# Kernel tuning notes

Hardware: AMD Instinct MI355X
Metric: run time of the kernel (lower is better)

Reference implementation:

```python
import jax, jax.numpy as jnp
import numpy as np

EPS = 1e-5

def conv3x3(x, w, b, stride=1):
    y = jax.lax.conv_general_dilated(x, w, (stride, stride), 'SAME',
                                     dimension_numbers=('NCHW', 'OIHW', 'NCHW'))
    return y + b[None, :, None, None]

def batchnorm_train(x, gamma, beta):
    # training-mode BN: batch statistics over (N, H, W)
    mean = x.mean(axis=(0, 2, 3), keepdims=True)
    var = x.var(axis=(0, 2, 3), keepdims=True)
    xh = (x - mean) * jax.lax.rsqrt(var + EPS)
    return xh * gamma[None, :, None, None] + beta[None, :, None, None]

def haar_dwt2(x):
    # pywt.dwt2(x, 'db1') on last two axes; even H,W so 'symmetric' padding is a no-op.
    # a = (x0 + x1)/sqrt2, d = (x0 - x1)/sqrt2 per axis -> 2x2 block combinations / 2.
    x00 = x[:, :, 0::2, 0::2]
    x01 = x[:, :, 0::2, 1::2]
    x10 = x[:, :, 1::2, 0::2]
    x11 = x[:, :, 1::2, 1::2]
    cA = (x00 + x01 + x10 + x11) * 0.5
    cH = (x00 + x01 - x10 - x11) * 0.5  # pywt 'da': detail along rows
    cV = (x00 - x01 + x10 - x11) * 0.5  # pywt 'ad': detail along cols
    cD = (x00 - x01 - x10 + x11) * 0.5
    return cA, cH, cV, cD


def setup_inputs() -> dict:
    key = jax.random.key(0)
    ks = jax.random.split(key, 8)
    N, in_c, out_c, H, W = 4, 3, 64, 512, 512

    def kaiming(k, shape):
        fan_in = shape[1] * shape[2] * shape[3]
        return jax.random.normal(k, shape, jnp.float32) * np.sqrt(2.0 / fan_in)

    inputs = jax.random.normal(ks[0], (N, in_c, H, W), jnp.float32)
    return {
        'inputs': inputs,
        # conv_block: conv1 -> bn1 -> conv2 -> bn2 -> relu
        'w1': kaiming(ks[1], (out_c, in_c, 3, 3)),
        'b1': jnp.zeros((out_c,), jnp.float32),
        'g1': jnp.ones((out_c,), jnp.float32),
        'be1': jnp.zeros((out_c,), jnp.float32),
        'w2': kaiming(ks[2], (out_c, out_c, 3, 3)),
        'b2': jnp.zeros((out_c,), jnp.float32),
        'g2': jnp.ones((out_c,), jnp.float32),
        'be2': jnp.zeros((out_c,), jnp.float32),
        # conv_dwt_block: conv(out_c*4 -> out_c) -> bn -> relu
        'w3': kaiming(ks[3], (out_c, out_c * 4, 3, 3)),
        'b3': jnp.zeros((out_c,), jnp.float32),
        'g3': jnp.ones((out_c,), jnp.float32),
        'be3': jnp.zeros((out_c,), jnp.float32),
    }


def reference(inputs, w1, b1, g1, be1, w2, b2, g2, be2, w3, b3, g3, be3):
    # conv_block
    x = conv3x3(inputs, w1, b1)
    x = batchnorm_train(x, g1, be1)
    x = conv3x3(x, w2, b2)
    x = batchnorm_train(x, g2, be2)
    skip_con = jax.nn.relu(x)

    # original detaches skip_con before the (CPU pywt) DWT -> no grad through this branch
    dwt_in = jax.lax.stop_gradient(skip_con)
    cA, cH, cV, cD = haar_dwt2(dwt_in)
    dwt = jnp.concatenate((cA, cH, cV, cD), axis=1)  # [N, 4*out_c, H/2, W/2]

    y = conv3x3(dwt, w3, b3)
    y = batchnorm_train(y, g3, be3)
    dwt_out = jax.nn.relu(y)
    return dwt_out, skip_con
```

## Files before the change

### kernel.cpp

```cpp
#include <hip/hip_runtime.h>
#include <cstdint>

typedef float f32x4 __attribute__((ext_vector_type(4)));
typedef __bf16 bf16x8 __attribute__((ext_vector_type(8)));
typedef unsigned int uint32;
typedef unsigned short ushort_t;

__device__ __forceinline__ ushort_t f2bf(float f) {
    uint32 u = __builtin_bit_cast(uint32, f);
    u = (u + 0x7fffu + ((u >> 16) & 1u)) >> 16;
    return (ushort_t)u;
}
__device__ __forceinline__ float bf2f(ushort_t h) {
    return __builtin_bit_cast(float, (uint32)h << 16);
}

__device__ __forceinline__ void gload_lds16(const void* g, void* l) {
    __builtin_amdgcn_global_load_lds(
        (const __attribute__((address_space(1))) uint32*)g,
        (__attribute__((address_space(3))) uint32*)l, 16, 0, 0);
}

__global__ __launch_bounds__(256) void im2col1_kernel(
    const float* __restrict__ in,
    ushort_t* __restrict__ P)
{
    int px = blockIdx.x * 256 + threadIdx.x;
    int n = px >> 18, rem = px & 262143;
    int y = rem >> 9, x = rem & 511;
    ushort_t pv[32];
#pragma unroll
    for (int ci = 0; ci < 3; ++ci)
#pragma unroll
        for (int t = 0; t < 9; ++t) {
            int dy = t / 3 - 1, dx = t % 3 - 1;
            int yy = y + dy, xx = x + dx;
            bool v = ((unsigned)yy < 512u) && ((unsigned)xx < 512u);
            pv[ci * 9 + t] = v ? f2bf(in[((n * 3 + ci) * 512 + yy) * 512 + xx])
                               : (ushort_t)0;
        }
#pragma unroll
    for (int k = 27; k < 32; ++k) pv[k] = 0;
    uint4* dst = (uint4*)(P + (size_t)px * 32);
    dst[0] = *(uint4*)(pv);
    dst[1] = *(uint4*)(pv + 8);
    dst[2] = *(uint4*)(pv + 16);
    dst[3] = *(uint4*)(pv + 24);
}

__global__ void prepw1_kernel(const float* __restrict__ w1,
                              ushort_t* __restrict__ Wsw1)
{
    int i = blockIdx.x * 256 + threadIdx.x;
    int ii = i & 7, lane = (i >> 3) & 63, nt = i >> 9;
    int cout = nt * 16 + (lane & 15);
    int k = (lane >> 4) * 8 + ii;
    Wsw1[i] = (k < 27) ? f2bf(w1[cout * 27 + k]) : (ushort_t)0;
}

__global__ __launch_bounds__(256) void gemm1_kernel(
    const ushort_t* __restrict__ P,
    const ushort_t* __restrict__ Wsw1,
    const float* __restrict__ b1,
    ushort_t* __restrict__ X1,
    float* __restrict__ stats)
{
    __shared__ float sred[4][128];
    int tid = threadIdx.x;
    int wave = tid >> 6, lane = tid & 63;
    int lp = lane & 15, lg = lane >> 4;
    int pxb = blockIdx.x * 256 + wave * 64;

    bf16x8 wf[4];
#pragma unroll
    for (int nt = 0; nt < 4; ++nt)
        wf[nt] = *(const bf16x8*)(Wsw1 + (nt * 64 + lane) * 8);

    f32x4 acc[4][4];
#pragma unroll
    for (int a = 0; a < 4; ++a)
#pragma unroll
        for (int b = 0; b < 4; ++b) acc[a][b] = (f32x4){0.f, 0.f, 0.f, 0.f};

#pragma unroll
    for (int nf = 0; nf < 4; ++nf) {
        bf16x8 bfrag = *(const bf16x8*)(P + (size_t)(pxb + nf * 16 + lp) * 32 + lg * 8);
#pragma unroll
        for (int nt = 0; nt < 4; ++nt)
            acc[nt][nf] = __builtin_amdgcn_mfma_f32_16x16x32_bf16(
                wf[nt], bfrag, acc[nt][nf], 0, 0, 0);
    }

    float s16[16], q16[16];
#pragma unroll
    for (int j = 0; j < 16; ++j) { s16[j] = 0.f; q16[j] = 0.f; }

#pragma unroll
    for (int nf = 0; nf < 4; ++nf) {
        size_t px = (size_t)pxb + nf * 16 + lp;
#pragma unroll
        for (int nt = 0; nt < 4; ++nt) {
            ushort_t ov[4];
#pragma unroll
            for (int r = 0; r < 4; ++r) {
                float o = acc[nt][nf][r] + b1[nt * 16 + lg * 4 + r];
                s16[nt * 4 + r] += o;
                q16[nt * 4 + r] += o * o;
                ov[r] = f2bf(o);
            }
            *(ushort4*)(X1 + px * 64 + nt * 16 + lg * 4) = *(ushort4*)ov;
        }
    }

#pragma unroll
    for (int off = 1; off < 16; off <<= 1)
#pragma unroll
        for (int j = 0; j < 16; ++j) {
            s16[j] += __shfl_xor(s16[j], off);
            q16[j] += __shfl_xor(q16[j], off);
        }
    if (lp == 0) {
#pragma unroll
        for (int nt = 0; nt < 4; ++nt)
#pragma unroll
            for (int r = 0; r < 4; ++r) {
                int ch = nt * 16 + lg * 4 + r;
                sred[wave][ch]      = s16[nt * 4 + r];
                sred[wave][64 + ch] = q16[nt * 4 + r];
            }
    }
    __syncthreads();
    if (tid < 128) {
        float tot = sred[0][tid] + sred[1][tid] + sred[2][tid] + sred[3][tid];
        atomicAdd(&stats[(blockIdx.x & 31) * 128 + tid], tot);
    }
}

__global__ void finalize_kernel(const float* __restrict__ stats,
                                const float* __restrict__ gamma,
                                const float* __restrict__ beta,
                                float inv_cnt, float* __restrict__ scsh)
{
    int c = threadIdx.x;
    float S = 0.f, Q = 0.f;
    for (int b = 0; b < 32; ++b) {
        S += stats[b * 128 + c];
        Q += stats[b * 128 + 64 + c];
    }
    float mean = S * inv_cnt;
    float var  = Q * inv_cnt - mean * mean;
    float rs   = rsqrtf(var + 1e-5f);
    float sc   = gamma[c] * rs;
    scsh[c]      = sc;
    scsh[64 + c] = beta[c] - mean * sc;
}

__global__ __launch_bounds__(256) void prepw_kernel(
    const float* __restrict__ w, const float* __restrict__ scale,
    ushort_t* __restrict__ Wsw, int CIN)
{
    int i = blockIdx.x * 256 + threadIdx.x;
    int KC = CIN >> 5;
    int ii = i & 7, lane = (i >> 3) & 63, nt = (i >> 9) & 3;
    int rest = i >> 11;
    int kc = rest % KC, t = rest / KC;
    if (t >= 9) return;
    int cout = nt * 16 + (lane & 15);
    int cin  = kc * 32 + (lane >> 4) * 8 + ii;
    float v = w[(cout * CIN + cin) * 9 + t];
    if (scale) v *= scale[cin];
    Wsw[i] = f2bf(v);
}

__global__ void prepT_kernel(const float* __restrict__ w2,
                             const float* __restrict__ shift,
                             float* __restrict__ T)
{
    int idx = threadIdx.x;
    if (idx < 576) {
        int t = idx / 64, cout = idx % 64;
        float s = 0.f;
        for (int cin = 0; cin < 64; ++cin)
            s += w2[(cout * 64 + cin) * 9 + t] * shift[cin];
        T[idx] = s;
    }
    __syncthreads();
    if (idx < 64) {
        float s = 0.f;
        for (int t = 0; t < 9; ++t) s += T[t * 64 + idx];
        T[576 + idx] = s;
    }
}

template <int CIN, bool HAS_T, int HH, int WW>
__global__ __launch_bounds__(256, 3) void conv_mfma5_kernel(
    const ushort_t* __restrict__ X,
    const ushort_t* __restrict__ Wsw,
    const float* __restrict__ T,
    const float* __restrict__ bias,
    ushort_t* __restrict__ Y,
    float* __restrict__ stats)
{
    constexpr int KC     = CIN >> 5;
    constexpr int COLS_B = WW >> 6;
    constexpr int ROWS_B = HH >> 2;

    __shared__ ushort_t tiles[2][12672];

    int nwg = gridDim.x;
    int bid = blockIdx.x;
    int cpx = nwg >> 3;
    int bs  = (bid & 7) * cpx + (bid >> 3);

    int tid  = threadIdx.x;
    int wave = tid >> 6, lane = tid & 63;
    int lp = lane & 15, lg = lane >> 4;

    int tmp = bs;
    int ctile = tmp % COLS_B;  tmp /= COLS_B;
    int rtile = tmp % ROWS_B;
    int n     = tmp / ROWS_B;
    int y0 = rtile << 2, x0 = ctile << 6;
    int y  = y0 + wave;

    uint32 goff[7];
    uint32 vmask = 0;
#pragma unroll
    for (int j = 0; j < 7; ++j) {
        int s = tid + j * 256;
        goff[j] = 0;
        if (s < 1584) {
            int plane = s / 396;
            int px    = s - plane * 396;
            int ry    = px / 66;
            int cx    = px - ry * 66;
            int gy = y0 - 1 + ry, gx = x0 - 1 + cx;
            if (((unsigned)gy < (unsigned)HH) && ((unsigned)gx < (unsigned)WW)) {
                vmask |= (1u << j);
                goff[j] = (uint32)((((uint32)(n * HH + gy) * WW + gx) * CIN
                                    + plane * 8) * 2);
            } else {
                uint4 zz; zz.x = zz.y = zz.z = zz.w = 0u;
                *(uint4*)((char*)tiles[0] + s * 16) = zz;
                *(uint4*)((char*)tiles[1] + s * 16) = zz;
            }
        }
    }

    const char* Xb = (const char*)X;
    auto stage = [&](int c, int b) {
        uint32 cofs = (uint32)c * 64u;
#pragma unroll
        for (int j = 0; j < 7; ++j) {
            if (vmask & (1u << j))
                gload_lds16(Xb + goff[j] + cofs,
                            (char*)tiles[b] + j * 4096 + wave * 1024);
        }
    };

    f32x4 acc[4][4];
#pragma unroll
    for (int a = 0; a < 4; ++a)
#pragma unroll
        for (int b = 0; b < 4; ++b) acc[a][b] = (f32x4){0.f, 0.f, 0.f, 0.f};

    stage(0, 0);
    __syncthreads();

#pragma unroll 1
    for (int c = 0; c < KC; ++c) {
        if (c + 1 < KC) stage(c + 1, (c + 1) & 1);
        const ushort_t* tile = tiles[c & 1];

#pragma unroll
        for (int t = 0; t < 9; ++t) {
            const int dy = t / 3 - 1, dx = t % 3 - 1;
            bf16x8 wf[4];
#pragma unroll
            for (int nt = 0; nt < 4; ++nt)
                wf[nt] = *(const bf16x8*)(Wsw + (size_t)(((t * KC + c) << 2) + nt) * 512 + lane * 8);
            int prow = (wave + 1 + dy) * 66 + (1 + dx) + lp;
#pragma unroll
            for (int nf = 0; nf < 4; ++nf) {
                int px = prow + nf * 16;
                bf16x8 bfrag = *(const bf16x8*)(tile + lg * 3168 + px * 8);
#pragma unroll
                for (int nt = 0; nt < 4; ++nt)
                    acc[nt][nf] = __builtin_amdgcn_mfma_f32_16x16x32_bf16(
                        wf[nt], bfrag, acc[nt][nf], 0, 0, 0);
            }
        }
        __syncthreads();
    }

    float (*sred)[128] = (float(*)[128])tiles[0];

    bool top = (y == 0), bot = (y == HH - 1);
    float s16[16], q16[16];
#pragma unroll
    for (int j = 0; j < 16; ++j) { s16[j] = 0.f; q16[j] = 0.f; }

    size_t rowbase = ((size_t)(n * HH + y) * WW) * 64;
#pragma unroll
    for (int nf = 0; nf < 4; ++nf) {
        int x = x0 + nf * 16 + lp;
        bool lft = (x == 0), rgt = (x == WW - 1);
        bool edge = top | bot | lft | rgt;
#pragma unroll
        for (int nt = 0; nt < 4; ++nt) {
            ushort_t ov[4];
#pragma unroll
            for (int r = 0; r < 4; ++r) {
                int ch = nt * 16 + lg * 4 + r;
                float o = acc[nt][nf][r] + bias[ch];
                if (HAS_T) {
                    o += T[576 + ch];
                    if (edge) {
#pragma unroll
                        for (int t = 0; t < 9; ++t) {
                            int dy = t / 3 - 1, dx = t % 3 - 1;
                            bool miss = (top && dy < 0) || (bot && dy > 0) ||
                                        (lft && dx < 0) || (rgt && dx > 0);
                            if (miss) o -= T[t * 64 + ch];
                        }
                    }
                }
                s16[nt * 4 + r] += o;
                q16[nt * 4 + r] += o * o;
                ov[r] = f2bf(o);
            }
            *(ushort4*)(Y + rowbase + (size_t)x * 64 + nt * 16 + lg * 4) = *(ushort4*)ov;
        }
    }

#pragma unroll
    for (int off = 1; off < 16; off <<= 1)
#pragma unroll
        for (int j = 0; j < 16; ++j) {
            s16[j] += __shfl_xor(s16[j], off);
            q16[j] += __shfl_xor(q16[j], off);
        }
    if (lp == 0) {
#pragma unroll
        for (int nt = 0; nt < 4; ++nt)
#pragma unroll
            for (int r = 0; r < 4; ++r) {
                int ch = nt * 16 + lg * 4 + r;
                sred[wave][ch]      = s16[nt * 4 + r];
                sred[wave][64 + ch] = q16[nt * 4 + r];
            }
    }
    __syncthreads();
    if (tid < 128) {
        float tot = sred[0][tid] + sred[1][tid] + sred[2][tid] + sred[3][tid];
        atomicAdd(&stats[(bs & 31) * 128 + tid], tot);
    }
}

__global__ __launch_bounds__(256) void bn2_dwt_skip_kernel(
    const ushort_t* __restrict__ X2, const float* __restrict__ scsh,
    float* __restrict__ skip,
    ushort_t* __restrict__ X3)
{
    __shared__ float v[128][65];
    int tid = threadIdx.x;
    int b = blockIdx.x;
    int n  = b >> 11;
    int r2 = b & 2047;
    int y0 = (r2 >> 3) << 1;
    int x0 = (r2 & 7) << 6;

#pragma unroll
    for (int k = 0; k < 4; ++k) {
        int q  = tid + k * 256;
        int px = q >> 3;
        int cb = (q & 7) * 8;
        int gy = y0 + (px >> 6);
        int gx = x0 + (px & 63);
        uint4 raw = *(const uint4*)(X2 + ((size_t)(n * 512 + gy) * 512 + gx) * 64 + cb);
        const ushort_t* up = (const ushort_t*)&raw;
#pragma unroll
        for (int j = 0; j < 8; ++j) {
            float f = bf2f(up[j]);
            float o = f * scsh[cb + j] + scsh[64 + cb + j];
            v[px][cb + j] = fmaxf(o, 0.f);
        }
    }
    __syncthreads();

    {
        int c = tid >> 2, sub = tid & 3;
#pragma unroll
        for (int rr = 0; rr < 2; ++rr) {
            float* orow = skip + ((size_t)(n * 64 + c) * 512 + (y0 + rr)) * 512 + x0;
#pragma unroll
            for (int qq = 0; qq < 4; ++qq) {
                int xb = qq * 16 + sub * 4;
                float4 w4;
                w4.x = v[rr * 64 + xb + 0][c];
                w4.y = v[rr * 64 + xb + 1][c];
                w4.z = v[rr * 64 + xb + 2][c];
                w4.w = v[rr * 64 + xb + 3][c];
                *(float4*)(orow + xb) = w4;
            }
        }
    }
    {
        int c = tid & 63, jj = tid >> 6;
        int yq = y0 >> 1, xq = x0 >> 1;
#pragma unroll
        for (int it = 0; it < 8; ++it) {
            int xl = jj * 8 + it;
            float x00 = v[2 * xl][c],      x01 = v[2 * xl + 1][c];
            float x10 = v[64 + 2 * xl][c], x11 = v[64 + 2 * xl + 1][c];
            float cA = (x00 + x01 + x10 + x11) * 0.5f;
            float cH = (x00 + x01 - x10 - x11) * 0.5f;
            float cV = (x00 - x01 + x10 - x11) * 0.5f;
            float cD = (x00 - x01 - x10 + x11) * 0.5f;
            ushort_t* dst = X3 + ((size_t)(n * 256 + yq) * 256 + xq + xl) * 256 + c;
            dst[0]   = f2bf(cA);
            dst[64]  = f2bf(cH);
            dst[128] = f2bf(cV);
            dst[192] = f2bf(cD);
        }
    }
}

__global__ __launch_bounds__(256) void bn3_kernel(
    const ushort_t* __restrict__ X4, const float* __restrict__ scsh,
    float* __restrict__ out)
{
    __shared__ float v[64][65];
    int tid = threadIdx.x;
    int b = blockIdx.x;
    int n  = b >> 10;
    int r2 = b & 1023;
    int y  = r2 >> 2;
    int x0 = (r2 & 3) << 6;

#pragma unroll
    for (int k = 0; k < 2; ++k) {
        int q  = tid + k * 256;
        int px = q >> 3;
        int cb = (q & 7) * 8;
        uint4 raw = *(const uint4*)(X4 + ((size_t)(n * 256 + y) * 256 + x0 + px) * 64 + cb);
        const ushort_t* up = (const ushort_t*)&raw;
#pragma unroll
        for (int j = 0; j < 8; ++j) {
            float f = bf2f(up[j]);
            float o = f * scsh[cb + j] + scsh[64 + cb + j];
            v[px][cb + j] = fmaxf(o, 0.f);
        }
    }
    __syncthreads();
    int c = tid >> 2, sub = tid & 3;
    float* orow = out + ((size_t)(n * 64 + c) * 256 + y) * 256 + x0;
#pragma unroll
    for (int qq = 0; qq < 4; ++qq) {
        int xb = qq * 16 + sub * 4;
        float4 w4;
        w4.x = v[xb + 0][c];
        w4.y = v[xb + 1][c];
        w4.z = v[xb + 2][c];
        w4.w = v[xb + 3][c];
        *(float4*)(orow + xb) = w4;
    }
}

extern "C" void kernel_launch(void* const* d_in, const int* in_sizes, int n_in,
                              void* d_out, int out_size, void* d_ws, size_t ws_size,
                              hipStream_t stream)
{
    const float* in  = (const float*)d_in[0];
    const float* w1  = (const float*)d_in[1];
    const float* b1  = (const float*)d_in[2];
    const float* g1  = (const float*)d_in[3];
    const float* be1 = (const float*)d_in[4];
    const float* w2  = (const float*)d_in[5];
    const float* b2  = (const float*)d_in[6];
    const float* g2  = (const float*)d_in[7];
    const float* be2 = (const float*)d_in[8];
    const float* w3  = (const float*)d_in[9];
    const float* b3  = (const float*)d_in[10];
    const float* g3  = (const float*)d_in[11];
    const float* be3 = (const float*)d_in[12];

    float* out     = (float*)d_out;
    float* dwt_out = out;
    float* skip    = out + 16777216;

    char* ws = (char*)d_ws;
    ushort_t* X1 = (ushort_t*)ws;
    ushort_t* X2 = (ushort_t*)(ws + 134217728);
    ushort_t* P  = X2;
    ushort_t* X3 = X1;
    ushort_t* X4 = X2;
    char* aux = ws + 268435456;
    float* stats1 = (float*)(aux);
    float* stats2 = (float*)(aux + 16384);
    float* stats3 = (float*)(aux + 32768);
    float* scsh1  = (float*)(aux + 49152);
    float* scsh2  = (float*)(aux + 49664);
    float* scsh3  = (float*)(aux + 50176);
    float* T2     = (float*)(aux + 50688);
    ushort_t* Wsw2 = (ushort_t*)(aux + 57344);
    ushort_t* Wsw3 = (ushort_t*)(aux + 131072);
    ushort_t* Wsw1 = (ushort_t*)(aux + 425984);

    hipMemsetAsync(aux, 0, 49152, stream);

    im2col1_kernel<<<4096, 256, 0, stream>>>(in, P);
    prepw1_kernel<<<8, 256, 0, stream>>>(w1, Wsw1);
    gemm1_kernel<<<4096, 256, 0, stream>>>(P, Wsw1, b1, X1, stats1);
    finalize_kernel<<<1, 64, 0, stream>>>(stats1, g1, be1, 1.f / 1048576.f, scsh1);
    prepw_kernel<<<144, 256, 0, stream>>>(w2, scsh1, Wsw2, 64);
    prepT_kernel<<<1, 576, 0, stream>>>(w2, scsh1 + 64, T2);

    conv_mfma5_kernel<64, true, 512, 512><<<4096, 256, 0, stream>>>(
        X1, Wsw2, T2, b2, X2, stats2);
    finalize_kernel<<<1, 64, 0, stream>>>(stats2, g2, be2, 1.f / 1048576.f, scsh2);

    bn2_dwt_skip_kernel<<<8192, 256, 0, stream>>>(X2, scsh2, skip, X3);

    prepw_kernel<<<576, 256, 0, stream>>>(w3, nullptr, Wsw3, 256);
    conv_mfma5_kernel<256, false, 256, 256><<<1024, 256, 0, stream>>>(
        X3, Wsw3, nullptr, b3, X4, stats3);
    finalize_kernel<<<1, 64, 0, stream>>>(stats3, g3, be3, 1.f / 262144.f, scsh3);

    bn3_kernel<<<4096, 256, 0, stream>>>(X4, scsh3, dwt_out);
}
```

Measured before the change: 594.1 us.

## Split conv tile into 2 rows by 2 channel halves, preload weights per chunk

The conv kernel now covers 2 output rows per block instead of 4. Each row is split between two waves, and each wave handles half of the 64 output channels. This shrinks the LDS tile and the accumulators, which should help occupancy, and doubles the grid. All nine taps' weight fragments are now loaded into registers before the stage of the next chunk is issued, instead of reloading weights per tap. The cost is more halo reloads per output row and duplicated B-fragment LDS reads across the channel halves.

Result: no change. 586.0 us (-1.4%).

```diff
diff --git a/kernel.cpp b/kernel.cpp
--- a/kernel.cpp
+++ b/kernel.cpp
@@ -193,7 +193,7 @@
 }
 
 template <int CIN, bool HAS_T, int HH, int WW>
-__global__ __launch_bounds__(256, 3) void conv_mfma5_kernel(
+__global__ __launch_bounds__(256, 3) void conv_mfma6_kernel(
     const ushort_t* __restrict__ X,
     const ushort_t* __restrict__ Wsw,
     const float* __restrict__ T,
@@ -203,9 +203,9 @@
 {
     constexpr int KC     = CIN >> 5;
     constexpr int COLS_B = WW >> 6;
-    constexpr int ROWS_B = HH >> 2;
-
-    __shared__ ushort_t tiles[2][12672];
+    constexpr int ROWS_B = HH >> 1;
+
+    __shared__ ushort_t tiles[2][8448];
 
     int nwg = gridDim.x;
     int bid = blockIdx.x;
@@ -215,23 +215,24 @@
     int tid  = threadIdx.x;
     int wave = tid >> 6, lane = tid & 63;
     int lp = lane & 15, lg = lane >> 4;
+    int row = wave >> 1, h = wave & 1;
 
     int tmp = bs;
     int ctile = tmp % COLS_B;  tmp /= COLS_B;
     int rtile = tmp % ROWS_B;
     int n     = tmp / ROWS_B;
-    int y0 = rtile << 2, x0 = ctile << 6;
-    int y  = y0 + wave;
-
-    uint32 goff[7];
+    int y0 = rtile << 1, x0 = ctile << 6;
+    int y  = y0 + row;
+
+    uint32 goff[5];
     uint32 vmask = 0;
 #pragma unroll
-    for (int j = 0; j < 7; ++j) {
+    for (int j = 0; j < 5; ++j) {
         int s = tid + j * 256;
         goff[j] = 0;
-        if (s < 1584) {
-            int plane = s / 396;
-            int px    = s - plane * 396;
+        if (s < 1056) {
+            int plane = s / 264;
+            int px    = s - plane * 264;
             int ry    = px / 66;
             int cx    = px - ry * 66;
             int gy = y0 - 1 + ry, gx = x0 - 1 + cx;
@@ -251,16 +252,16 @@
     auto stage = [&](int c, int b) {
         uint32 cofs = (uint32)c * 64u;
 #pragma unroll
-        for (int j = 0; j < 7; ++j) {
+        for (int j = 0; j < 5; ++j) {
             if (vmask & (1u << j))
                 gload_lds16(Xb + goff[j] + cofs,
                             (char*)tiles[b] + j * 4096 + wave * 1024);
         }
     };
 
-    f32x4 acc[4][4];
-#pragma unroll
-    for (int a = 0; a < 4; ++a)
+    f32x4 acc[2][4];
+#pragma unroll
+    for (int a = 0; a < 2; ++a)
 #pragma unroll
         for (int b = 0; b < 4; ++b) acc[a][b] = (f32x4){0.f, 0.f, 0.f, 0.f};
 
@@ -269,25 +270,29 @@
 
 #pragma unroll 1
     for (int c = 0; c < KC; ++c) {
+        bf16x8 wreg[9][2];
+#pragma unroll
+        for (int t = 0; t < 9; ++t)
+#pragma unroll
+            for (int ntl = 0; ntl < 2; ++ntl)
+                wreg[t][ntl] = *(const bf16x8*)(
+                    Wsw + (size_t)(((t * KC + c) << 2) + (h * 2 + ntl)) * 512 + lane * 8);
+        __builtin_amdgcn_sched_barrier(0);
         if (c + 1 < KC) stage(c + 1, (c + 1) & 1);
+
         const ushort_t* tile = tiles[c & 1];
-
 #pragma unroll
         for (int t = 0; t < 9; ++t) {
             const int dy = t / 3 - 1, dx = t % 3 - 1;
-            bf16x8 wf[4];
-#pragma unroll
-            for (int nt = 0; nt < 4; ++nt)
-                wf[nt] = *(const bf16x8*)(Wsw + (size_t)(((t * KC + c) << 2) + nt) * 512 + lane * 8);
-            int prow = (wave + 1 + dy) * 66 + (1 + dx) + lp;
+            int prow = (row + 1 + dy) * 66 + (1 + dx) + lp;
 #pragma unroll
             for (int nf = 0; nf < 4; ++nf) {
                 int px = prow + nf * 16;
-                bf16x8 bfrag = *(const bf16x8*)(tile + lg * 3168 + px * 8);
-#pragma unroll
-                for (int nt = 0; nt < 4; ++nt)
-                    acc[nt][nf] = __builtin_amdgcn_mfma_f32_16x16x32_bf16(
-                        wf[nt], bfrag, acc[nt][nf], 0, 0, 0);
+                bf16x8 bfrag = *(const bf16x8*)(tile + lg * 2112 + px * 8);
+                acc[0][nf] = __builtin_amdgcn_mfma_f32_16x16x32_bf16(
+                    wreg[t][0], bfrag, acc[0][nf], 0, 0, 0);
+                acc[1][nf] = __builtin_amdgcn_mfma_f32_16x16x32_bf16(
+                    wreg[t][1], bfrag, acc[1][nf], 0, 0, 0);
             }
         }
         __syncthreads();
@@ -296,9 +301,9 @@
     float (*sred)[128] = (float(*)[128])tiles[0];
 
     bool top = (y == 0), bot = (y == HH - 1);
-    float s16[16], q16[16];
-#pragma unroll
-    for (int j = 0; j < 16; ++j) { s16[j] = 0.f; q16[j] = 0.f; }
+    float s8[8], q8[8];
+#pragma unroll
+    for (int j = 0; j < 8; ++j) { s8[j] = 0.f; q8[j] = 0.f; }
 
     size_t rowbase = ((size_t)(n * HH + y) * WW) * 64;
 #pragma unroll
@@ -307,12 +312,12 @@
         bool lft = (x == 0), rgt = (x == WW - 1);
         bool edge = top | bot | lft | rgt;
 #pragma unroll
-        for (int nt = 0; nt < 4; ++nt) {
+        for (int ntl = 0; ntl < 2; ++ntl) {
             ushort_t ov[4];
 #pragma unroll
             for (int r = 0; r < 4; ++r) {
-                int ch = nt * 16 + lg * 4 + r;
-                float o = acc[nt][nf][r] + bias[ch];
+                int ch = (h * 2 + ntl) * 16 + lg * 4 + r;
+                float o = acc[ntl][nf][r] + bias[ch];
                 if (HAS_T) {
                     o += T[576 + ch];
                     if (edge) {
@@ -325,34 +330,37 @@
                         }
                     }
                 }
-                s16[nt * 4 + r] += o;
-                q16[nt * 4 + r] += o * o;
+                s8[ntl * 4 + r] += o;
+                q8[ntl * 4 + r] += o * o;
                 ov[r] = f2bf(o);
             }
-            *(ushort4*)(Y + rowbase + (size_t)x * 64 + nt * 16 + lg * 4) = *(ushort4*)ov;
+            *(ushort4*)(Y + rowbase + (size_t)x * 64 + (h * 2 + ntl) * 16 + lg * 4)
+                = *(ushort4*)ov;
         }
     }
 
 #pragma unroll
     for (int off = 1; off < 16; off <<= 1)
 #pragma unroll
-        for (int j = 0; j < 16; ++j) {
-            s16[j] += __shfl_xor(s16[j], off);
-            q16[j] += __shfl_xor(q16[j], off);
+        for (int j = 0; j < 8; ++j) {
+            s8[j] += __shfl_xor(s8[j], off);
+            q8[j] += __shfl_xor(q8[j], off);
         }
     if (lp == 0) {
 #pragma unroll
-        for (int nt = 0; nt < 4; ++nt)
+        for (int ntl = 0; ntl < 2; ++ntl)
 #pragma unroll
             for (int r = 0; r < 4; ++r) {
-                int ch = nt * 16 + lg * 4 + r;
-                sred[wave][ch]      = s16[nt * 4 + r];
-                sred[wave][64 + ch] = q16[nt * 4 + r];
+                int ch = (h * 2 + ntl) * 16 + lg * 4 + r;
+                sred[wave][ch]      = s8[ntl * 4 + r];
+                sred[wave][64 + ch] = q8[ntl * 4 + r];
             }
     }
     __syncthreads();
     if (tid < 128) {
-        float tot = sred[0][tid] + sred[1][tid] + sred[2][tid] + sred[3][tid];
+        int ch = tid & 63;
+        int h2 = ch >> 5;
+        float tot = sred[h2][tid] + sred[2 + h2][tid];
         atomicAdd(&stats[(bs & 31) * 128 + tid], tot);
     }
 }
@@ -516,14 +524,14 @@
     prepw_kernel<<<144, 256, 0, stream>>>(w2, scsh1, Wsw2, 64);
     prepT_kernel<<<1, 576, 0, stream>>>(w2, scsh1 + 64, T2);
 
-    conv_mfma5_kernel<64, true, 512, 512><<<4096, 256, 0, stream>>>(
+    conv_mfma6_kernel<64, true, 512, 512><<<8192, 256, 0, stream>>>(
         X1, Wsw2, T2, b2, X2, stats2);
     finalize_kernel<<<1, 64, 0, stream>>>(stats2, g2, be2, 1.f / 1048576.f, scsh2);
 
     bn2_dwt_skip_kernel<<<8192, 256, 0, stream>>>(X2, scsh2, skip, X3);
 
     prepw_kernel<<<576, 256, 0, stream>>>(w3, nullptr, Wsw3, 256);
-    conv_mfma5_kernel<256, false, 256, 256><<<1024, 256, 0, stream>>>(
+    conv_mfma6_kernel<256, false, 256, 256><<<2048, 256, 0, stream>>>(
         X3, Wsw3, nullptr, b3, X4, stats3);
     finalize_kernel<<<1, 64, 0, stream>>>(stats3, g3, be3, 1.f / 262144.f, scsh3);
 
```

## Stage conv weights into LDS alongside activation tiles with dynamic shared memory

Applied to the files above, without the earlier changes.

The conv kernel now loads weight fragments for each input-channel chunk into double-buffered LDS using global_load_lds, instead of reading them per wave from global memory. Shared memory becomes dynamic (about 124 KB) and launch bounds drop to one block per CU. The aim is to cut repeated global/L2 weight traffic and its latency inside the MFMA loop. The cost is much lower occupancy, which leaves less latency hiding for the activation loads.

Result: slower. 750.6 us (+26.3%).

```diff
diff --git a/kernel.cpp b/kernel.cpp
--- a/kernel.cpp
+++ b/kernel.cpp
@@ -193,7 +193,7 @@
 }
 
 template <int CIN, bool HAS_T, int HH, int WW>
-__global__ __launch_bounds__(256, 3) void conv_mfma5_kernel(
+__global__ __launch_bounds__(256, 1) void conv_mfma7_kernel(
     const ushort_t* __restrict__ X,
     const ushort_t* __restrict__ Wsw,
     const float* __restrict__ T,
@@ -205,7 +205,7 @@
     constexpr int COLS_B = WW >> 6;
     constexpr int ROWS_B = HH >> 2;
 
-    __shared__ ushort_t tiles[2][12672];
+    extern __shared__ char smem[];
 
     int nwg = gridDim.x;
     int bid = blockIdx.x;
@@ -215,6 +215,7 @@
     int tid  = threadIdx.x;
     int wave = tid >> 6, lane = tid & 63;
     int lp = lane & 15, lg = lane >> 4;
+    int wbase16 = (tid & 192) * 16;
 
     int tmp = bs;
     int ctile = tmp % COLS_B;  tmp /= COLS_B;
@@ -223,12 +224,12 @@
     int y0 = rtile << 2, x0 = ctile << 6;
     int y  = y0 + wave;
 
-    uint32 goff[7];
-    uint32 vmask = 0;
+    uint32 agoff[7];
+    uint32 amask = 0;
 #pragma unroll
     for (int j = 0; j < 7; ++j) {
         int s = tid + j * 256;
-        goff[j] = 0;
+        agoff[j] = 0;
         if (s < 1584) {
             int plane = s / 396;
             int px    = s - plane * 396;
@@ -236,25 +237,33 @@
             int cx    = px - ry * 66;
             int gy = y0 - 1 + ry, gx = x0 - 1 + cx;
             if (((unsigned)gy < (unsigned)HH) && ((unsigned)gx < (unsigned)WW)) {
-                vmask |= (1u << j);
-                goff[j] = (uint32)((((uint32)(n * HH + gy) * WW + gx) * CIN
-                                    + plane * 8) * 2);
+                amask |= (1u << j);
+                agoff[j] = (uint32)((((uint32)(n * HH + gy) * WW + gx) * CIN
+                                     + plane * 8) * 2);
             } else {
                 uint4 zz; zz.x = zz.y = zz.z = zz.w = 0u;
-                *(uint4*)((char*)tiles[0] + s * 16) = zz;
-                *(uint4*)((char*)tiles[1] + s * 16) = zz;
-            }
-        }
-    }
-
+                *(uint4*)(smem + s * 16)         = zz;
+                *(uint4*)(smem + 25344 + s * 16) = zz;
+            }
+        }
+    }
     const char* Xb = (const char*)X;
-    auto stage = [&](int c, int b) {
-        uint32 cofs = (uint32)c * 64u;
+    const char* Wb = (const char*)Wsw;
+
+    auto stage = [&](int c) {
+        char* ab = smem + (c & 1) * 25344;
+        char* wb = smem + 50688 + (c & 1) * 36864;
+        uint32 ca = (uint32)c * 64u;
+        uint32 cw = (uint32)c * 4096u;
 #pragma unroll
         for (int j = 0; j < 7; ++j) {
-            if (vmask & (1u << j))
-                gload_lds16(Xb + goff[j] + cofs,
-                            (char*)tiles[b] + j * 4096 + wave * 1024);
+            if (amask & (1u << j))
+                gload_lds16(Xb + agoff[j] + ca, ab + j * 4096 + wbase16);
+        }
+#pragma unroll
+        for (int j = 0; j < 9; ++j) {
+            gload_lds16(Wb + (uint32)(j * KC) * 4096u + cw + (uint32)tid * 16u,
+                        wb + j * 4096 + wbase16);
         }
     };
 
@@ -264,13 +273,14 @@
 #pragma unroll
         for (int b = 0; b < 4; ++b) acc[a][b] = (f32x4){0.f, 0.f, 0.f, 0.f};
 
-    stage(0, 0);
+    stage(0);
     __syncthreads();
 
 #pragma unroll 1
     for (int c = 0; c < KC; ++c) {
-        if (c + 1 < KC) stage(c + 1, (c + 1) & 1);
-        const ushort_t* tile = tiles[c & 1];
+        if (c + 1 < KC) stage(c + 1);
+        const char* ab = smem + (c & 1) * 25344;
+        const char* wb = smem + 50688 + (c & 1) * 36864;
 
 #pragma unroll
         for (int t = 0; t < 9; ++t) {
@@ -278,12 +288,12 @@
             bf16x8 wf[4];
 #pragma unroll
             for (int nt = 0; nt < 4; ++nt)
-                wf[nt] = *(const bf16x8*)(Wsw + (size_t)(((t * KC + c) << 2) + nt) * 512 + lane * 8);
+                wf[nt] = *(const bf16x8*)(wb + ((t * 4 + nt) * 64 + lane) * 16);
             int prow = (wave + 1 + dy) * 66 + (1 + dx) + lp;
 #pragma unroll
             for (int nf = 0; nf < 4; ++nf) {
                 int px = prow + nf * 16;
-                bf16x8 bfrag = *(const bf16x8*)(tile + lg * 3168 + px * 8);
+                bf16x8 bfrag = *(const bf16x8*)(ab + lg * 6336 + px * 16);
 #pragma unroll
                 for (int nt = 0; nt < 4; ++nt)
                     acc[nt][nf] = __builtin_amdgcn_mfma_f32_16x16x32_bf16(
@@ -293,7 +303,7 @@
         __syncthreads();
     }
 
-    float (*sred)[128] = (float(*)[128])tiles[0];
+    float (*sred)[128] = (float(*)[128])(smem + 50688);
 
     bool top = (y == 0), bot = (y == HH - 1);
     float s16[16], q16[16];
@@ -507,6 +517,14 @@
     ushort_t* Wsw3 = (ushort_t*)(aux + 131072);
     ushort_t* Wsw1 = (ushort_t*)(aux + 425984);
 
+    constexpr int kSmem = 124416;
+    hipFuncSetAttribute(
+        reinterpret_cast<const void*>(&conv_mfma7_kernel<64, true, 512, 512>),
+        hipFuncAttributeMaxDynamicSharedMemorySize, kSmem);
+    hipFuncSetAttribute(
+        reinterpret_cast<const void*>(&conv_mfma7_kernel<256, false, 256, 256>),
+        hipFuncAttributeMaxDynamicSharedMemorySize, kSmem);
+
     hipMemsetAsync(aux, 0, 49152, stream);
 
     im2col1_kernel<<<4096, 256, 0, stream>>>(in, P);
@@ -516,14 +534,14 @@
     prepw_kernel<<<144, 256, 0, stream>>>(w2, scsh1, Wsw2, 64);
     prepT_kernel<<<1, 576, 0, stream>>>(w2, scsh1 + 64, T2);
 
-    conv_mfma5_kernel<64, true, 512, 512><<<4096, 256, 0, stream>>>(
+    conv_mfma7_kernel<64, true, 512, 512><<<4096, 256, kSmem, stream>>>(
         X1, Wsw2, T2, b2, X2, stats2);
     finalize_kernel<<<1, 64, 0, stream>>>(stats2, g2, be2, 1.f / 1048576.f, scsh2);
 
     bn2_dwt_skip_kernel<<<8192, 256, 0, stream>>>(X2, scsh2, skip, X3);
 
     prepw_kernel<<<576, 256, 0, stream>>>(w3, nullptr, Wsw3, 256);
-    conv_mfma5_kernel<256, false, 256, 256><<<1024, 256, 0, stream>>>(
+    conv_mfma7_kernel<256, false, 256, 256><<<1024, 256, kSmem, stream>>>(
         X3, Wsw3, nullptr, b3, X4, stats3);
     finalize_kernel<<<1, 64, 0, stream>>>(stats3, g3, be3, 1.f / 262144.f, scsh3);
 
```
